# Kernel tuning notes

Hardware: AMD Instinct MI355X
Metric: run time of the kernel (lower is better)

Reference implementation:

```python
import jax, jax.numpy as jnp
import numpy as np

N = 4096          # total ensemble boxes per frame
M = 20            # MAX_MERGE_NUMS
H = 16            # MergeNet hidden_c
COND_THRES = 0.2
IOU_THRES = 0.3


def setup_inputs() -> dict:
    key = jax.random.key(0)
    ks = jax.random.split(key, 6)
    u = jax.random.uniform(ks[0], (N, 9), dtype=jnp.float32)
    # realistic lidar boxes: centers in a ~140x80x8m range, dims in [0.5, 4.5), heading in [-pi, pi)
    centers = (u[:, 0:3] - 0.5) * jnp.array([140.0, 80.0, 8.0], jnp.float32)
    dims = u[:, 3:6] * 4.0 + 0.5
    heading = (u[:, 6:7] - 0.5) * (2.0 * np.pi)
    extra = u[:, 7:9]  # extra box attrs (cols 7:9), untouched by merge
    pred_boxes = jnp.concatenate([centers, dims, heading, extra], axis=-1)
    pred_scores = jax.random.uniform(ks[1], (N,), dtype=jnp.float32)
    pred_labels = jax.random.randint(ks[2], (N,), 0, 3)
    w1 = (jax.random.normal(ks[3], (M, H), jnp.float32) / np.sqrt(M)).astype(jnp.float32)
    b1 = jnp.zeros((H,), jnp.float32)
    w2 = (jax.random.normal(ks[4], (H, H), jnp.float32) / np.sqrt(H)).astype(jnp.float32)
    b2 = jnp.zeros((H,), jnp.float32)
    w3 = (jax.random.normal(ks[5], (H, 1), jnp.float32) / np.sqrt(H)).astype(jnp.float32)
    b3 = jnp.zeros((1,), jnp.float32)
    return dict(pred_boxes=pred_boxes, pred_scores=pred_scores, pred_labels=pred_labels,
                w1=w1, b1=b1, w2=w2, b2=b2, w3=w3, b3=b3)


def _bev_aligned(b):
    # boxes3d_lidar_to_aligned_bev_boxes: swap dx/dy when |limit_period(heading)| >= pi/4
    ang = b[..., 6] - jnp.floor(b[..., 6] / np.pi + 0.5) * np.pi
    swap = jnp.abs(ang) >= (np.pi / 4)
    dx = jnp.where(swap, b[..., 4], b[..., 3])
    dy = jnp.where(swap, b[..., 3], b[..., 4])
    return jnp.stack([b[..., 0] - dx / 2, b[..., 1] - dy / 2,
                      b[..., 0] + dx / 2, b[..., 1] + dy / 2], axis=-1)


def _iou_one_many(a, b):
    # axis-aligned BEV IoU of one box a[4] vs many b[N,4]
    xmin = jnp.maximum(a[0], b[:, 0]); ymin = jnp.maximum(a[1], b[:, 1])
    xmax = jnp.minimum(a[2], b[:, 2]); ymax = jnp.minimum(a[3], b[:, 3])
    inter = jnp.maximum(xmax - xmin, 0.0) * jnp.maximum(ymax - ymin, 0.0)
    area_a = (a[2] - a[0]) * (a[3] - a[1])
    area_b = (b[:, 2] - b[:, 0]) * (b[:, 3] - b[:, 1])
    return inter / jnp.maximum(area_a + area_b - inter, 1e-6)


def _nms_merge(pred_boxes, pred_scores, pred_labels, w1, b1, w2, b2, w3, b3):
    valid = pred_scores > COND_THRES
    sort_key = jnp.where(valid, pred_scores, -jnp.inf)
    order = jnp.argsort(-sort_key)                 # descending by score; invalid sink
    boxes9 = pred_boxes[order]
    labels = pred_labels[order]
    scores = pred_scores[order]
    suppressed0 = ~valid[order]
    boxes7 = boxes9[:, :7]
    bev0 = _bev_aligned(boxes7)                    # merged boxes get suppressed, so bev is static

    def mergenet(ob):                              # ob: [M, 7] -> merged box [7]
        x = ob.T                                   # [7, M] (k is the feature axis)
        h = jax.nn.relu(x @ w1 + b1)
        h = jax.nn.relu(h @ w2 + b2)
        return (h @ w3 + b3)[:, 0]

    def step(suppressed, i):
        active = ~suppressed[i]
        same = (labels == labels[i]) & (~suppressed)
        iou = _iou_one_many(bev0[i], bev0)         # [N]
        over = (iou > IOU_THRES) & same            # includes self (iou=1)
        count = jnp.sum(over)
        rank = jnp.cumsum(over) - 1                # slot of each overlap, in score order
        tgt = jnp.where(over & (rank < M), rank, M)
        ob = jnp.zeros((M, 7), boxes7.dtype).at[tgt].set(boxes7, mode='drop')
        bi = boxes7[i]
        new_box = jnp.where(count > 1, mergenet(ob), bi)
        new_box = new_box.at[3:6].set(jnp.maximum(new_box[3:6], 1e-5))
        out_box = jnp.where(active, new_box, bi)
        return suppressed | (over & active), (out_box, active)

    _, (merged7, keep) = jax.lax.scan(step, suppressed0, jnp.arange(N))
    out_boxes = jnp.concatenate([merged7, boxes9[:, 7:9]], axis=-1)   # [N, 9]
    return out_boxes, scores, labels, keep


def reference(pred_boxes, pred_scores, pred_labels, w1, b1, w2, b2, w3, b3):
    # Returns fixed-shape (boxes9, scores, labels, keep_mask); rows with keep=False
    # correspond to boxes that torch's dynamic version would have removed.
    return _nms_merge(pred_boxes, pred_scores, pred_labels, w1, b1, w2, b2, w3, b3)
```

## Files before the change

kernel.cpp:

```cpp
#include <hip/hip_runtime.h>
#include <cstdint>

typedef unsigned long long u64;
typedef unsigned int u32;

#define NB 4096
#define NW 64
#define MM 20
#define HH 16
#define COND_THRES 0.2f
#define IOU_THRES 0.3f
#define PI_F  3.14159265358979323846f
#define PI4_F 0.78539816339744830962f

#define WS_KEPT    0
#define WS_MASK    32768
#define WS_BOX9S   (WS_MASK + NB*NW*8)
#define WS_BEVS    (WS_BOX9S + NB*9*4)
#define WS_SCORES  (WS_BEVS + NB*16)
#define WS_LABELS  (WS_SCORES + NB*4)
#define WS_NBRW    (WS_LABELS + NB*4)

__device__ __forceinline__ u64 sort_key(float s, int i) {
  u32 sb = (s > COND_THRES) ? __float_as_uint(s) : 0u;
  return ((u64)(sb ^ 0xFFFFFFFFu) << 12) | (u64)i;
}

__global__ void __launch_bounds__(256) k_prep(const float* __restrict__ scores,
                                              const float* __restrict__ boxes9,
                                              const int* __restrict__ labels,
                                              float* __restrict__ box9s, float4* __restrict__ bevs,
                                              float* __restrict__ scoress, int* __restrict__ labelss,
                                              u64* __restrict__ nbrw) {
  #pragma clang fp contract(off)
  __shared__ u64 keys[NB];
  __shared__ u32 part[16][16];
  int tid = threadIdx.x;
  for (int k = tid; k < NB; k += 256) keys[k] = sort_key(scores[k], k);
  __syncthreads();
  int bl = tid & 15;
  int ch = tid >> 4;
  u64 ki = keys[blockIdx.x * 16 + bl];
  int c = 0;
  #pragma unroll 16
  for (int t = 0; t < 256; ++t) c += (keys[(ch << 8) + t] < ki) ? 1 : 0;
  part[bl][ch] = (u32)c;
  __syncthreads();
  if (tid < 16) {
    int i = blockIdx.x * 16 + tid;
    int r = 0;
    #pragma unroll
    for (int q = 0; q < 16; ++q) r += (int)part[tid][q];
    nbrw[i] = 0;
    float b[9];
    #pragma unroll
    for (int f = 0; f < 9; ++f) b[f] = boxes9[i * 9 + f];
    #pragma unroll
    for (int f = 0; f < 9; ++f) box9s[r * 9 + f] = b[f];
    float ang = b[6] - floorf(b[6] / PI_F + 0.5f) * PI_F;
    bool sw = fabsf(ang) >= PI4_F;
    float dx = sw ? b[4] : b[3];
    float dy = sw ? b[3] : b[4];
    bevs[r] = make_float4(b[0] - dx * 0.5f, b[1] - dy * 0.5f,
                          b[0] + dx * 0.5f, b[1] + dy * 0.5f);
    scoress[r] = scores[i];
    labelss[r] = labels[i];
  }
}

__global__ void __launch_bounds__(64) k_mask(const float4* __restrict__ bevs,
                                             const int* __restrict__ labelss,
                                             const float* __restrict__ scoress,
                                             u64* __restrict__ mask,
                                             u64* __restrict__ nbrw) {
  #pragma clang fp contract(off)
  __shared__ float4 bj[64];
  __shared__ int lj[64];
  int t = threadIdx.x;
  int jt = blockIdx.x;
  int it = blockIdx.y;
  int j = jt * 64 + t;
  bj[t] = bevs[j];
  lj[t] = labelss[j];
  u64 vj = __ballot(scoress[j] > COND_THRES);
  int i = it * 64 + t;
  float4 a = bevs[i];
  int la = labelss[i];
  float area_a = (a.z - a.x) * (a.w - a.y);
  __syncthreads();
  u64 w = 0;
  #pragma unroll 8
  for (int kk = 0; kk < 64; ++kk) {
    float4 bb = bj[kk];
    float xmin = fmaxf(a.x, bb.x), ymin = fmaxf(a.y, bb.y);
    float xmax = fminf(a.z, bb.z), ymax = fminf(a.w, bb.w);
    float inter = fmaxf(xmax - xmin, 0.0f) * fmaxf(ymax - ymin, 0.0f);
    float area_b = (bb.z - bb.x) * (bb.w - bb.y);
    float iou = inter / fmaxf(area_a + area_b - inter, 1e-6f);
    if ((iou > IOU_THRES) && (la == lj[kk])) w |= (1ull << kk);
  }
  mask[(u64)i * NW + jt] = w;
  if (jt <= it) {
    u64 below = (jt < it) ? ~0ull : ((1ull << t) - 1ull);
    if (w & vj & below) atomicOr(&nbrw[i], 1ull << jt);
  }
}

__global__ void __launch_bounds__(1024) k_nms(const u64* __restrict__ mask,
                                              const u64* __restrict__ nbrw,
                                              const float* __restrict__ scoress,
                                              u64* __restrict__ keptOut) {
  __shared__ u64 csL[NB];
  __shared__ u64 ce0L[NB];
  __shared__ u64 ce1L[NB];
  __shared__ u64 remL[NB];
  __shared__ u32 emL[NB];
  __shared__ u64 vwL[64];
  int tid = threadIdx.x;
  int lane = tid & 63;
  int waveId = tid >> 6;
  #pragma unroll
  for (int s4 = 0; s4 < 4; ++s4) {
    int i = tid + (s4 << 10);
    bool v = scoress[i] > COND_THRES;
    u64 vb = __ballot(v);
    if (lane == 0) vwL[waveId + (s4 << 4)] = vb;
  }
  #pragma unroll
  for (int s4 = 0; s4 < 4; ++s4) {
    int i = tid + (s4 << 10);
    int wi = i >> 6;
    u64 bit = 1ull << (i & 63);
    u64 t = nbrw[i];
    u64 cs = 0, c0 = 0, c1 = 0, rem = 0;
    u32 i0 = 0, i1 = 0; int n = 0;
    while (t) {
      int w = __builtin_ctzll(t);
      t &= t - 1;
      u64 m = mask[(u64)i * NW + w];
      if (w == wi) {
        cs = m & (bit - 1ull);
      } else {
        if (n == 0)      { c0 = m; i0 = (u32)w; }
        else if (n == 1) { c1 = m; i1 = (u32)w; }
        else rem |= 1ull << w;
        ++n;
      }
    }
    csL[i] = cs; ce0L[i] = c0; ce1L[i] = c1; remL[i] = rem;
    emL[i] = i0 | (i1 << 6);
  }
  __syncthreads();
  if (tid < 64) {
    u64 keptW = 0;
    u64 cs_c = csL[lane], ce0_c = ce0L[lane], ce1_c = ce1L[lane], rem_c = remL[lane];
    u32 em_c = emL[lane];
    u64 vws_c = vwL[0];
    for (int s = 0; s < 64; ++s) {
      u64 cs_n = 0, ce0_n = 0, ce1_n = 0, rem_n = 0, vws_n = 0; u32 em_n = 0;
      if (s < 63) {
        int ip = ((s + 1) << 6) | lane;
        cs_n = csL[ip]; ce0_n = ce0L[ip]; ce1_n = ce1L[ip];
        rem_n = remL[ip]; em_n = emL[ip]; vws_n = vwL[s + 1];
      }
      int w0 = (int)(em_c & 63u), w1 = (int)((em_c >> 6) & 63u);
      u64 k0 = __shfl(keptW, w0);
      u64 k1 = __shfl(keptW, w1);
      bool hk = ((ce0_c & k0) | (ce1_c & k1)) != 0ull;
      u64 rem = rem_c;
      while (__ballot(rem != 0ull) != 0ull) {
        int w = rem ? __builtin_ctzll(rem) : 0;
        u64 kws = __shfl(keptW, w);
        if (rem) {
          u64 m = mask[(u64)((s << 6) | lane) * NW + w];
          hk = hk || ((m & kws) != 0ull);
          rem &= rem - 1;
        }
      }
      u64 dw = ~vws_c;
      u64 kw = 0;
      bool und = (vws_c >> lane) & 1ull;
      while (true) {
        bool dec = und && ((cs_c & ~dw) == 0ull);
        bool keep = dec && !hk && ((cs_c & kw) == 0ull);
        dw |= __ballot(dec);
        kw |= __ballot(keep);
        und = und && !dec;
        if (__ballot(und) == 0ull) break;
      }
      if (lane == s) keptW = kw;
      cs_c = cs_n; ce0_c = ce0_n; ce1_c = ce1_n; rem_c = rem_n; em_c = em_n; vws_c = vws_n;
    }
    keptOut[lane] = keptW;
  }
}

__global__ void __launch_bounds__(64) k_merge(
    const u64* __restrict__ mask, const u64* __restrict__ keptG,
    const float* __restrict__ box9s, const float* __restrict__ scoress,
    const int* __restrict__ labelss,
    const float* __restrict__ w1, const float* __restrict__ b1,
    const float* __restrict__ w2, const float* __restrict__ b2,
    const float* __restrict__ w3, const float* __restrict__ b3,
    float* __restrict__ out) {
  #pragma clang fp contract(off)
  __shared__ int candList[MM];
  __shared__ float ob[MM][7];
  __shared__ float h1[7][HH];
  __shared__ float h2[7][HH];
  __shared__ float res[7];
  __shared__ u64 K[64];
  int i = blockIdx.x;
  int t = threadIdx.x;
  K[t] = keptG[t];
  __syncthreads();
  bool active = (K[i >> 6] >> (i & 63)) & 1ull;
  u64 wq = 0;
  int cnt = 0;
  if (active) {
    u64 w = mask[(u64)i * NW + t];
    int hiw = i >> 6;
    u64 below = (1ull << (i & 63)) - 1ull;
    while (w) {
      int b = __builtin_ctzll(w);
      w &= w - 1;
      int j = (t << 6) | b;
      if (scoress[j] > COND_THRES) {
        const u64* rowj = mask + (u64)j * NW;
        u64 found = rowj[hiw] & K[hiw] & below;
        for (int ww = 0; ww < hiw; ++ww) found |= rowj[ww] & K[ww];
        if (!found) { wq |= (1ull << b); cnt++; }
      }
    }
  }
  int incl = cnt;
  #pragma unroll
  for (int off = 1; off < 64; off <<= 1) {
    int v = __shfl_up(incl, off);
    if (t >= off) incl += v;
  }
  int excl = incl - cnt;
  int count = __shfl(incl, 63);
  bool merged = active && (count > 1);
  if (merged && wq) {
    int pos = excl;
    u64 ww = wq;
    while (ww && pos < MM) {
      int b = __builtin_ctzll(ww);
      ww &= ww - 1;
      candList[pos++] = (t << 6) | b;
    }
  }
  __syncthreads();
  if (merged) {
    int nc = count < MM ? count : MM;
    if (t < MM) {
      if (t < nc) {
        int j = candList[t];
        #pragma unroll
        for (int f = 0; f < 7; ++f) ob[t][f] = box9s[j * 9 + f];
      } else {
        #pragma unroll
        for (int f = 0; f < 7; ++f) ob[t][f] = 0.0f;
      }
    }
    __syncthreads();
    for (int o = t; o < 7 * HH; o += 64) {
      int f = o >> 4, hh = o & 15;
      float acc = b1[hh];
      #pragma unroll
      for (int m = 0; m < MM; ++m) acc += ob[m][f] * w1[m * HH + hh];
      h1[f][hh] = fmaxf(acc, 0.0f);
    }
    __syncthreads();
    for (int o = t; o < 7 * HH; o += 64) {
      int f = o >> 4, oo = o & 15;
      float acc = b2[oo];
      #pragma unroll
      for (int k = 0; k < HH; ++k) acc += h1[f][k] * w2[k * HH + oo];
      h2[f][oo] = fmaxf(acc, 0.0f);
    }
    __syncthreads();
    if (t < 7) {
      float acc = b3[0];
      #pragma unroll
      for (int k = 0; k < HH; ++k) acc += h2[t][k] * w3[k];
      if (t >= 3 && t < 6) acc = fmaxf(acc, 1e-5f);
      res[t] = acc;
    }
    __syncthreads();
  }
  if (t < 9) {
    float v = box9s[i * 9 + t];
    if (merged && t < 7) v = res[t];
    out[i * 9 + t] = v;
  }
  if (t == 0) {
    out[NB * 9 + i]          = scoress[i];
    out[NB * 9 + NB + i]     = (float)labelss[i];
    out[NB * 9 + 2 * NB + i] = active ? 1.0f : 0.0f;
  }
}

extern "C" void kernel_launch(void* const* d_in, const int* in_sizes, int n_in,
                              void* d_out, int out_size, void* d_ws, size_t ws_size,
                              hipStream_t stream) {
  const float* boxes9 = (const float*)d_in[0];
  const float* scores = (const float*)d_in[1];
  const int*   labels = (const int*)d_in[2];
  const float* w1 = (const float*)d_in[3];
  const float* b1 = (const float*)d_in[4];
  const float* w2 = (const float*)d_in[5];
  const float* b2 = (const float*)d_in[6];
  const float* w3 = (const float*)d_in[7];
  const float* b3 = (const float*)d_in[8];
  char* ws = (char*)d_ws;
  u64*    kept    = (u64*)(ws + WS_KEPT);
  u64*    mask    = (u64*)(ws + WS_MASK);
  float*  box9s   = (float*)(ws + WS_BOX9S);
  float4* bevs    = (float4*)(ws + WS_BEVS);
  float*  scoress = (float*)(ws + WS_SCORES);
  int*    labelss = (int*)(ws + WS_LABELS);
  u64*    nbrw    = (u64*)(ws + WS_NBRW);
  float*  out     = (float*)d_out;

  hipLaunchKernelGGL(k_prep,  dim3(256),    dim3(256),  0, stream,
                     scores, boxes9, labels, box9s, bevs, scoress, labelss, nbrw);
  hipLaunchKernelGGL(k_mask,  dim3(64, 64), dim3(64),   0, stream,
                     bevs, labelss, scoress, mask, nbrw);
  hipLaunchKernelGGL(k_nms,   dim3(1),      dim3(1024), 0, stream,
                     mask, nbrw, scoress, kept);
  hipLaunchKernelGGL(k_merge, dim3(NB),     dim3(64),   0, stream,
                     mask, kept, box9s, scoress, labelss,
                     w1, b1, w2, b2, w3, b3, out);
}
```

Measured before the change: 131.3 us.

## Exploit mask symmetry, precompute suppressor step, and simplify merge overlap check

The IoU mask kernel now computes only lower-triangular tiles (2080 blocks) and fills the upper tiles by transposing each tile through shared memory. It also records the first two cross-tile neighbour words per row with atomics, so the NMS kernel no longer scans the mask. The NMS kernel additionally computes, for every box, the index of its earliest kept suppressor. This lets the merge kernel test overlap candidates with a single lookup instead of rescanning mask rows against the kept words. The cost is extra atomics, tile transposes, a serial tail in the single-block NMS kernel, and the triangular-index arithmetic.

```diff
diff --git a/kernel.cpp b/kernel.cpp
--- a/kernel.cpp
+++ b/kernel.cpp
@@ -13,13 +13,19 @@
 #define PI_F  3.14159265358979323846f
 #define PI4_F 0.78539816339744830962f
 
-#define WS_KEPT    0
+#define NTILE 2080
+
 #define WS_MASK    32768
 #define WS_BOX9S   (WS_MASK + NB*NW*8)
 #define WS_BEVS    (WS_BOX9S + NB*9*4)
 #define WS_SCORES  (WS_BEVS + NB*16)
 #define WS_LABELS  (WS_SCORES + NB*4)
 #define WS_NBRW    (WS_LABELS + NB*4)
+#define WS_SUPSTEP (WS_NBRW + NB*8)
+#define WS_CNT     (WS_SUPSTEP + NB*4)
+#define WS_SLOTW   (WS_CNT + NB*4)
+#define WS_SLOTI   (WS_SLOTW + NB*16)
+#define WS_CSARR   (WS_SLOTI + NB*8)
 
 __device__ __forceinline__ u64 sort_key(float s, int i) {
   u32 sb = (s > COND_THRES) ? __float_as_uint(s) : 0u;
@@ -31,7 +37,7 @@
                                               const int* __restrict__ labels,
                                               float* __restrict__ box9s, float4* __restrict__ bevs,
                                               float* __restrict__ scoress, int* __restrict__ labelss,
-                                              u64* __restrict__ nbrw) {
+                                              u64* __restrict__ nbrw, u32* __restrict__ cnt) {
   #pragma clang fp contract(off)
   __shared__ u64 keys[NB];
   __shared__ u32 part[16][16];
@@ -52,6 +58,7 @@
     #pragma unroll
     for (int q = 0; q < 16; ++q) r += (int)part[tid][q];
     nbrw[i] = 0;
+    cnt[i] = 0;
     float b[9];
     #pragma unroll
     for (int f = 0; f < 9; ++f) b[f] = boxes9[i * 9 + f];
@@ -72,13 +79,21 @@
                                              const int* __restrict__ labelss,
                                              const float* __restrict__ scoress,
                                              u64* __restrict__ mask,
-                                             u64* __restrict__ nbrw) {
+                                             u64* __restrict__ nbrw,
+                                             u32* __restrict__ cnt,
+                                             u64* __restrict__ slotW,
+                                             u32* __restrict__ slotI,
+                                             u64* __restrict__ csArr) {
   #pragma clang fp contract(off)
   __shared__ float4 bj[64];
   __shared__ int lj[64];
+  __shared__ u64 tw[64];
   int t = threadIdx.x;
-  int jt = blockIdx.x;
-  int it = blockIdx.y;
+  int b = blockIdx.x;
+  int it = (int)((sqrtf(8.0f * (float)b + 1.0f) - 1.0f) * 0.5f);
+  while ((it + 1) * (it + 2) / 2 <= b) ++it;
+  while (it * (it + 1) / 2 > b) --it;
+  int jt = b - it * (it + 1) / 2;
   int j = jt * 64 + t;
   bj[t] = bevs[j];
   lj[t] = labelss[j];
@@ -100,22 +115,40 @@
     if ((iou > IOU_THRES) && (la == lj[kk])) w |= (1ull << kk);
   }
   mask[(u64)i * NW + jt] = w;
-  if (jt <= it) {
-    u64 below = (jt < it) ? ~0ull : ((1ull << t) - 1ull);
-    if (w & vj & below) atomicOr(&nbrw[i], 1ull << jt);
+  if (jt == it) {
+    csArr[i] = w & ((1ull << t) - 1ull);
+  } else {
+    if (w & vj) {
+      u32 pos = atomicAdd(&cnt[i], 1u);
+      if (pos < 2u) { slotW[i * 2 + pos] = w; slotI[i * 2 + pos] = (u32)jt; }
+      atomicOr(&nbrw[i], 1ull << jt);
+    }
+  }
+  if (jt < it) {
+    tw[t] = w;
+    __syncthreads();
+    u64 wT = 0;
+    #pragma unroll 8
+    for (int k = 0; k < 64; ++k) wT |= ((tw[k] >> t) & 1ull) << k;
+    mask[(u64)j * NW + it] = wT;
   }
 }
 
 __global__ void __launch_bounds__(1024) k_nms(const u64* __restrict__ mask,
                                               const u64* __restrict__ nbrw,
+                                              const u32* __restrict__ cnt,
+                                              const u64* __restrict__ slotW,
+                                              const u32* __restrict__ slotI,
+                                              const u64* __restrict__ csArr,
                                               const float* __restrict__ scoress,
-                                              u64* __restrict__ keptOut) {
+                                              int* __restrict__ supstep) {
   __shared__ u64 csL[NB];
-  __shared__ u64 ce0L[NB];
-  __shared__ u64 ce1L[NB];
+  __shared__ u64 c0L[NB];
+  __shared__ u64 c1L[NB];
   __shared__ u64 remL[NB];
-  __shared__ u32 emL[NB];
+  __shared__ u32 i01L[NB];
   __shared__ u64 vwL[64];
+  __shared__ u64 keptL[64];
   int tid = threadIdx.x;
   int lane = tid & 63;
   int waveId = tid >> 6;
@@ -129,44 +162,35 @@
   #pragma unroll
   for (int s4 = 0; s4 < 4; ++s4) {
     int i = tid + (s4 << 10);
-    int wi = i >> 6;
-    u64 bit = 1ull << (i & 63);
-    u64 t = nbrw[i];
-    u64 cs = 0, c0 = 0, c1 = 0, rem = 0;
-    u32 i0 = 0, i1 = 0; int n = 0;
-    while (t) {
-      int w = __builtin_ctzll(t);
-      t &= t - 1;
-      u64 m = mask[(u64)i * NW + w];
-      if (w == wi) {
-        cs = m & (bit - 1ull);
-      } else {
-        if (n == 0)      { c0 = m; i0 = (u32)w; }
-        else if (n == 1) { c1 = m; i1 = (u32)w; }
-        else rem |= 1ull << w;
-        ++n;
-      }
-    }
-    csL[i] = cs; ce0L[i] = c0; ce1L[i] = c1; remL[i] = rem;
-    emL[i] = i0 | (i1 << 6);
+    u32 c = cnt[i];
+    u64 c0 = 0, c1 = 0; u32 i0 = 0, i1 = 0;
+    if (c >= 1u) { c0 = slotW[i * 2];     i0 = slotI[i * 2]; }
+    if (c >= 2u) { c1 = slotW[i * 2 + 1]; i1 = slotI[i * 2 + 1]; }
+    u32 n = c > 2u ? 2u : c;
+    u32 ovf = c > 2u ? 1u : 0u;
+    u64 rem = 0;
+    if (ovf) rem = nbrw[i] & ~(1ull << i0) & ~(1ull << i1);
+    csL[i] = csArr[i];
+    c0L[i] = c0; c1L[i] = c1; remL[i] = rem;
+    i01L[i] = i0 | (i1 << 6) | (n << 12) | (ovf << 14);
   }
   __syncthreads();
   if (tid < 64) {
     u64 keptW = 0;
-    u64 cs_c = csL[lane], ce0_c = ce0L[lane], ce1_c = ce1L[lane], rem_c = remL[lane];
-    u32 em_c = emL[lane];
+    u64 cs_c = csL[lane], c0_c = c0L[lane], c1_c = c1L[lane], rem_c = remL[lane];
+    u32 m_c = i01L[lane];
     u64 vws_c = vwL[0];
     for (int s = 0; s < 64; ++s) {
-      u64 cs_n = 0, ce0_n = 0, ce1_n = 0, rem_n = 0, vws_n = 0; u32 em_n = 0;
+      u64 cs_n = 0, c0_n = 0, c1_n = 0, rem_n = 0, vws_n = 0; u32 m_n = 0;
       if (s < 63) {
         int ip = ((s + 1) << 6) | lane;
-        cs_n = csL[ip]; ce0_n = ce0L[ip]; ce1_n = ce1L[ip];
-        rem_n = remL[ip]; em_n = emL[ip]; vws_n = vwL[s + 1];
-      }
-      int w0 = (int)(em_c & 63u), w1 = (int)((em_c >> 6) & 63u);
+        cs_n = csL[ip]; c0_n = c0L[ip]; c1_n = c1L[ip];
+        rem_n = remL[ip]; m_n = i01L[ip]; vws_n = vwL[s + 1];
+      }
+      int w0 = (int)(m_c & 63u), w1 = (int)((m_c >> 6) & 63u);
       u64 k0 = __shfl(keptW, w0);
       u64 k1 = __shfl(keptW, w1);
-      bool hk = ((ce0_c & k0) | (ce1_c & k1)) != 0ull;
+      bool hk = ((c0_c & k0) | (c1_c & k1)) != 0ull;
       u64 rem = rem_c;
       while (__ballot(rem != 0ull) != 0ull) {
         int w = rem ? __builtin_ctzll(rem) : 0;
@@ -189,14 +213,59 @@
         if (__ballot(und) == 0ull) break;
       }
       if (lane == s) keptW = kw;
-      cs_c = cs_n; ce0_c = ce0_n; ce1_c = ce1_n; rem_c = rem_n; em_c = em_n; vws_c = vws_n;
-    }
-    keptOut[lane] = keptW;
+      cs_c = cs_n; c0_c = c0_n; c1_c = c1_n; rem_c = rem_n; m_c = m_n; vws_c = vws_n;
+    }
+    keptL[lane] = keptW;
+  }
+  __syncthreads();
+  #pragma unroll
+  for (int s4 = 0; s4 < 4; ++s4) {
+    int j = tid + (s4 << 10);
+    int wj = j >> 6;
+    bool valid = (vwL[wj] >> (j & 63)) & 1ull;
+    int res;
+    if (!valid) {
+      res = -1;
+    } else {
+      res = j;
+      u32 m = i01L[j];
+      u64 cs = csL[j];
+      int cand = 0x7FFFFFFF;
+      if (!(m & (1u << 14))) {
+        u32 n = (m >> 12) & 3;
+        if (n >= 1) {
+          int w0 = (int)(m & 63u);
+          u64 h = c0L[j] & keptL[w0];
+          if (h) { int r = (w0 << 6) + __builtin_ctzll(h); if (r < cand) cand = r; }
+        }
+        if (n >= 2) {
+          int w1 = (int)((m >> 6) & 63u);
+          u64 h = c1L[j] & keptL[w1];
+          if (h) { int r = (w1 << 6) + __builtin_ctzll(h); if (r < cand) cand = r; }
+        }
+        { u64 h = cs & keptL[wj];
+          if (h) { int r = (wj << 6) + __builtin_ctzll(h); if (r < cand) cand = r; } }
+      } else {
+        u64 t = nbrw[j];
+        while (t) {
+          int w = __builtin_ctzll(t);
+          t &= t - 1;
+          u64 h = mask[(u64)j * NW + w] & keptL[w];
+          if (h) { cand = (w << 6) + __builtin_ctzll(h); break; }
+        }
+        if (cand == 0x7FFFFFFF) {
+          u64 h = cs & keptL[wj];
+          if (h) cand = (wj << 6) + __builtin_ctzll(h);
+        }
+      }
+      if (cand != 0x7FFFFFFF) res = cand;
+    }
+    supstep[j] = res;
   }
 }
 
 __global__ void __launch_bounds__(64) k_merge(
-    const u64* __restrict__ mask, const u64* __restrict__ keptG,
+    const u64* __restrict__ mask, const int* __restrict__ supstep,
     const float* __restrict__ box9s, const float* __restrict__ scoress,
     const int* __restrict__ labelss,
     const float* __restrict__ w1, const float* __restrict__ b1,
@@ -209,28 +278,18 @@
   __shared__ float h1[7][HH];
   __shared__ float h2[7][HH];
   __shared__ float res[7];
-  __shared__ u64 K[64];
   int i = blockIdx.x;
   int t = threadIdx.x;
-  K[t] = keptG[t];
-  __syncthreads();
-  bool active = (K[i >> 6] >> (i & 63)) & 1ull;
+  bool active = (supstep[i] == i);
   u64 wq = 0;
   int cnt = 0;
   if (active) {
     u64 w = mask[(u64)i * NW + t];
-    int hiw = i >> 6;
-    u64 below = (1ull << (i & 63)) - 1ull;
     while (w) {
       int b = __builtin_ctzll(w);
       w &= w - 1;
       int j = (t << 6) | b;
-      if (scoress[j] > COND_THRES) {
-        const u64* rowj = mask + (u64)j * NW;
-        u64 found = rowj[hiw] & K[hiw] & below;
-        for (int ww = 0; ww < hiw; ++ww) found |= rowj[ww] & K[ww];
-        if (!found) { wq |= (1ull << b); cnt++; }
-      }
+      if (supstep[j] >= i) { wq |= (1ull << b); cnt++; }
     }
   }
   int incl = cnt;
@@ -315,22 +374,26 @@
   const float* w3 = (const float*)d_in[7];
   const float* b3 = (const float*)d_in[8];
   char* ws = (char*)d_ws;
-  u64*    kept    = (u64*)(ws + WS_KEPT);
   u64*    mask    = (u64*)(ws + WS_MASK);
   float*  box9s   = (float*)(ws + WS_BOX9S);
   float4* bevs    = (float4*)(ws + WS_BEVS);
   float*  scoress = (float*)(ws + WS_SCORES);
   int*    labelss = (int*)(ws + WS_LABELS);
   u64*    nbrw    = (u64*)(ws + WS_NBRW);
+  int*    supstep = (int*)(ws + WS_SUPSTEP);
+  u32*    cnt     = (u32*)(ws + WS_CNT);
+  u64*    slotW   = (u64*)(ws + WS_SLOTW);
+  u32*    slotI   = (u32*)(ws + WS_SLOTI);
+  u64*    csArr   = (u64*)(ws + WS_CSARR);
   float*  out     = (float*)d_out;
 
-  hipLaunchKernelGGL(k_prep,  dim3(256),    dim3(256),  0, stream,
-                     scores, boxes9, labels, box9s, bevs, scoress, labelss, nbrw);
-  hipLaunchKernelGGL(k_mask,  dim3(64, 64), dim3(64),   0, stream,
-                     bevs, labelss, scoress, mask, nbrw);
-  hipLaunchKernelGGL(k_nms,   dim3(1),      dim3(1024), 0, stream,
-                     mask, nbrw, scoress, kept);
-  hipLaunchKernelGGL(k_merge, dim3(NB),     dim3(64),   0, stream,
-                     mask, kept, box9s, scoress, labelss,
+  hipLaunchKernelGGL(k_prep,  dim3(256),   dim3(256),  0, stream,
+                     scores, boxes9, labels, box9s, bevs, scoress, labelss, nbrw, cnt);
+  hipLaunchKernelGGL(k_mask,  dim3(NTILE), dim3(64),   0, stream,
+                     bevs, labelss, scoress, mask, nbrw, cnt, slotW, slotI, csArr);
+  hipLaunchKernelGGL(k_nms,   dim3(1),     dim3(1024), 0, stream,
+                     mask, nbrw, cnt, slotW, slotI, csArr, scoress, supstep);
+  hipLaunchKernelGGL(k_merge, dim3(NB),    dim3(64),   0, stream,
+                     mask, supstep, box9s, scoress, labelss,
                      w1, b1, w2, b2, w3, b3, out);
 }
```

Result: faster. 125.4 us (-4.5%).
